# Kernel tuning notes

Measured on AMD Instinct MI355X. Metric: run time of the kernel, lower is better.

The kernel has to match this reference:

```python
import jax, jax.numpy as jnp
import numpy as np

B, T, C, H = 256, 256, 1024, 64

def setup_inputs() -> dict:
    key = jax.random.key(0)
    kx, kk, kq, kv = jax.random.split(key, 4)
    x = jax.random.normal(kx, (B, T, C), dtype=jnp.float32)
    # Dense kernels init'd with normal(stddev=0.02), stored as [in, out] like flax
    Wk = jax.random.normal(kk, (C, H), dtype=jnp.float32) * 0.02
    Wq = jax.random.normal(kq, (C, H), dtype=jnp.float32) * 0.02
    Wv = jax.random.normal(kv, (C, H), dtype=jnp.float32) * 0.02
    return {"x": x, "Wk": Wk, "Wq": Wq, "Wv": Wv}

def reference(x, Wk, Wq, Wv):
    # single-head causal self-attention (eval mode: dropout is identity)
    k = jnp.einsum('btc,ch->bth', x, Wk)      # [B,T,H]
    q = jnp.einsum('btc,ch->bth', x, Wq)      # [B,T,H]
    v = jnp.einsum('btc,ch->bth', x, Wv)      # [B,T,H]
    scale = jnp.asarray(k.shape[-1], k.dtype) ** -0.5
    wei = jnp.einsum('bth,bsh->bts', q, k) * scale  # [B,T,T]
    t = x.shape[1]
    causal = jnp.tril(jnp.ones((t, t), dtype=bool))
    wei = jnp.where(causal, wei, -jnp.inf)
    wei = jax.nn.softmax(wei, axis=-1)
    out = jnp.einsum('bts,bsh->bth', wei, v)  # [B,T,H]
    return out
```

## Files before the change

kernel.cpp:

```cpp
#include <hip/hip_runtime.h>

typedef float f32x4 __attribute__((ext_vector_type(4)));
typedef short s16x8 __attribute__((ext_vector_type(8)));

#define MFMA16 __builtin_amdgcn_mfma_f32_16x16x32_bf16

typedef const __attribute__((address_space(1))) void* gptr_t;
typedef __attribute__((address_space(3))) void* lptr_t;

__device__ __forceinline__ unsigned short f2bf(float f) {
    union { float f; unsigned u; } v; v.f = f;
    unsigned r = v.u + 0x7FFF + ((v.u >> 16) & 1);
    return (unsigned short)(r >> 16);
}

__global__ void prep_w(const float* __restrict__ Wk, const float* __restrict__ Wq,
                       const float* __restrict__ Wv, unsigned short* __restrict__ wt) {
    int n = blockIdx.x;
    int tid = threadIdx.x;
    const float* src; int col; float sc = 1.0f;
    if (n < 64)       { src = Wq; col = n;       sc = 0.125f; }
    else if (n < 128) { src = Wk; col = n - 64; }
    else              { src = Wv; col = n - 128; }
#pragma unroll
    for (int i = 0; i < 4; i++) {
        int c = i * 256 + tid;
        wt[n * 1024 + c] = f2bf(src[c * 64 + col] * sc);
    }
}

__global__ __launch_bounds__(512, 2) void fused_kernel(const float* __restrict__ x,
                                                       const unsigned short* __restrict__ wt,
                                                       float* __restrict__ out) {
    __shared__ unsigned short smem[2 * 256 * 72 + 64 * 264 + 8 * 16 * 56];
    unsigned short* Ql  = smem;
    unsigned short* Kl  = smem + 256 * 72;
    unsigned short* Vt  = smem + 2 * 256 * 72;
    unsigned short* Pl8 = smem + 2 * 256 * 72 + 64 * 264;
    unsigned short* Wl  = smem;

    const int tid  = threadIdx.x;
    const int lane = tid & 63;
    const int wid  = tid >> 6;
    const int quad = lane >> 4;
    const int l15  = lane & 15;
    const int b    = blockIdx.x;
    const int m0   = wid * 32;

    const float* xb  = x + (long)b * 256 * 1024;
    const float* ar0 = xb + (long)(m0 + l15) * 1024 + quad * 8;
    const float* ar1 = ar0 + 16 * 1024;

    const int srow = wid * 24 + (lane >> 3);
    const int cswz = (lane & 7) ^ (srow & 7);

    const unsigned short* wbase0 = Wl + l15 * 64 + ((0 + quad) ^ (l15 & 7)) * 8;
    const unsigned short* wbase1 = Wl + l15 * 64 + ((4 + quad) ^ (l15 & 7)) * 8;

    f32x4 acc[2][12] = {};

    for (int t = 0; t < 16; t++) {
        const int k0 = t * 64;
        if (t) __syncthreads();
#pragma unroll
        for (int j = 0; j < 3; j++) {
            const unsigned short* src = wt + (long)(srow + j * 8) * 1024 + k0 + cswz * 8;
            unsigned short* dst = Wl + (wid * 24 + j * 8) * 64;
            __builtin_amdgcn_global_load_lds((gptr_t)src, (lptr_t)dst, 16, 0, 0);
        }
        float4 px0 = *(const float4*)(ar0 + k0);
        float4 px1 = *(const float4*)(ar0 + k0 + 4);
        float4 px2 = *(const float4*)(ar0 + k0 + 32);
        float4 px3 = *(const float4*)(ar0 + k0 + 36);
        float4 px4 = *(const float4*)(ar1 + k0);
        float4 px5 = *(const float4*)(ar1 + k0 + 4);
        float4 px6 = *(const float4*)(ar1 + k0 + 32);
        float4 px7 = *(const float4*)(ar1 + k0 + 36);
        __syncthreads();

#pragma unroll
        for (int kk = 0; kk < 64; kk += 32) {
            s16x8 bfv[12];
            const unsigned short* wb = (kk == 0) ? wbase0 : wbase1;
#pragma unroll
            for (int nt = 0; nt < 12; nt++)
                bfv[nt] = *(const s16x8*)(wb + nt * 1024);

            s16x8 af0, af1;
            if (kk == 0) {
                af0 = s16x8{ (short)f2bf(px0.x), (short)f2bf(px0.y), (short)f2bf(px0.z), (short)f2bf(px0.w),
                             (short)f2bf(px1.x), (short)f2bf(px1.y), (short)f2bf(px1.z), (short)f2bf(px1.w) };
                af1 = s16x8{ (short)f2bf(px4.x), (short)f2bf(px4.y), (short)f2bf(px4.z), (short)f2bf(px4.w),
                             (short)f2bf(px5.x), (short)f2bf(px5.y), (short)f2bf(px5.z), (short)f2bf(px5.w) };
            } else {
                af0 = s16x8{ (short)f2bf(px2.x), (short)f2bf(px2.y), (short)f2bf(px2.z), (short)f2bf(px2.w),
                             (short)f2bf(px3.x), (short)f2bf(px3.y), (short)f2bf(px3.z), (short)f2bf(px3.w) };
                af1 = s16x8{ (short)f2bf(px6.x), (short)f2bf(px6.y), (short)f2bf(px6.z), (short)f2bf(px6.w),
                             (short)f2bf(px7.x), (short)f2bf(px7.y), (short)f2bf(px7.z), (short)f2bf(px7.w) };
            }
#pragma unroll
            for (int nt = 0; nt < 12; nt++) {
                acc[0][nt] = MFMA16(af0, bfv[nt], acc[0][nt], 0, 0, 0);
                acc[1][nt] = MFMA16(af1, bfv[nt], acc[1][nt], 0, 0, 0);
            }
        }
    }
    __syncthreads();

#pragma unroll
    for (int mt = 0; mt < 2; mt++) {
#pragma unroll
        for (int nt = 0; nt < 12; nt++) {
            if (nt < 4) {
#pragma unroll
                for (int r = 0; r < 4; r++)
                    Ql[(m0 + mt * 16 + quad * 4 + r) * 72 + nt * 16 + l15] = f2bf(acc[mt][nt][r]);
            } else if (nt < 8) {
#pragma unroll
                for (int r = 0; r < 4; r++)
                    Kl[(m0 + mt * 16 + quad * 4 + r) * 72 + (nt - 4) * 16 + l15] = f2bf(acc[mt][nt][r]);
            } else {
                ushort4 pv;
                pv.x = f2bf(acc[mt][nt][0]); pv.y = f2bf(acc[mt][nt][1]);
                pv.z = f2bf(acc[mt][nt][2]); pv.w = f2bf(acc[mt][nt][3]);
                *(ushort4*)&Vt[((nt - 8) * 16 + l15) * 264 + m0 + mt * 16 + quad * 4] = pv;
            }
        }
    }
    __syncthreads();

    unsigned short* Pw = Pl8 + wid * (16 * 56);

#pragma unroll
    for (int ti = 0; ti < 2; ti++) {
        const int r0 = (ti == 0 ? wid : 15 - wid) * 16;

        s16x8 qf0 = *(const s16x8*)&Ql[(r0 + l15) * 72 + quad * 8];
        s16x8 qf1 = *(const s16x8*)&Ql[(r0 + l15) * 72 + 32 + quad * 8];

        f32x4 o[4] = {};
        float mr[4], lr[4];
#pragma unroll
        for (int r = 0; r < 4; r++) { mr[r] = -1e30f; lr[r] = 0.0f; }

        const int nst = (r0 >> 5) + 1;
        for (int st = 0; st < nst; st++) {
            const int s0 = st * 32;
            s16x8 kf00 = *(const s16x8*)&Kl[(s0 + l15) * 72 + quad * 8];
            s16x8 kf01 = *(const s16x8*)&Kl[(s0 + l15) * 72 + 32 + quad * 8];
            s16x8 kf10 = *(const s16x8*)&Kl[(s0 + 16 + l15) * 72 + quad * 8];
            s16x8 kf11 = *(const s16x8*)&Kl[(s0 + 16 + l15) * 72 + 32 + quad * 8];
            s16x8 vf[4];
#pragma unroll
            for (int n = 0; n < 4; n++)
                vf[n] = *(const s16x8*)&Vt[(n * 16 + l15) * 264 + s0 + quad * 8];

            f32x4 S0 = {0.f, 0.f, 0.f, 0.f}, S1 = {0.f, 0.f, 0.f, 0.f};
            S0 = MFMA16(qf0, kf00, S0, 0, 0, 0);
            S0 = MFMA16(qf1, kf01, S0, 0, 0, 0);
            S1 = MFMA16(qf0, kf10, S1, 0, 0, 0);
            S1 = MFMA16(qf1, kf11, S1, 0, 0, 0);

            if (s0 + 31 > r0) {
#pragma unroll
                for (int r = 0; r < 4; r++) {
                    int t = r0 + quad * 4 + r;
                    if (s0 + l15 > t)      S0[r] = -1e30f;
                    if (s0 + 16 + l15 > t) S1[r] = -1e30f;
                }
            }

            float a4[4];
#pragma unroll
            for (int r = 0; r < 4; r++) {
                float rm = fmaxf(S0[r], S1[r]);
                rm = fmaxf(rm, __shfl_xor(rm, 1));
                rm = fmaxf(rm, __shfl_xor(rm, 2));
                rm = fmaxf(rm, __shfl_xor(rm, 4));
                rm = fmaxf(rm, __shfl_xor(rm, 8));
                float mn = fmaxf(mr[r], rm);
                float al = exp2f((mr[r] - mn) * 1.44269504f);
                mr[r] = mn;
                float p0 = exp2f((S0[r] - mn) * 1.44269504f);
                float p1 = exp2f((S1[r] - mn) * 1.44269504f);
                float rs = p0 + p1;
                rs += __shfl_xor(rs, 1);
                rs += __shfl_xor(rs, 2);
                rs += __shfl_xor(rs, 4);
                rs += __shfl_xor(rs, 8);
                lr[r] = al * lr[r] + rs;
                a4[r] = al;
                Pw[(quad * 4 + r) * 56 + l15]      = f2bf(p0);
                Pw[(quad * 4 + r) * 56 + l15 + 16] = f2bf(p1);
            }
#pragma unroll
            for (int n = 0; n < 4; n++) {
                f32x4 tt = o[n];
#pragma unroll
                for (int r = 0; r < 4; r++) tt[r] *= a4[r];
                o[n] = tt;
            }
            s16x8 pf = *(const s16x8*)&Pw[l15 * 56 + quad * 8];
#pragma unroll
            for (int n = 0; n < 4; n++)
                o[n] = MFMA16(pf, vf[n], o[n], 0, 0, 0);
        }

        float inv[4];
#pragma unroll
        for (int r = 0; r < 4; r++) inv[r] = 1.0f / lr[r];
#pragma unroll
        for (int n = 0; n < 4; n++)
#pragma unroll
            for (int r = 0; r < 4; r++) {
                long t = (long)b * 256 + r0 + quad * 4 + r;
                out[t * 64 + n * 16 + l15] = o[n][r] * inv[r];
            }
    }
}

extern "C" void kernel_launch(void* const* d_in, const int* in_sizes, int n_in,
                              void* d_out, int out_size, void* d_ws, size_t ws_size,
                              hipStream_t stream) {
    const float* x  = (const float*)d_in[0];
    const float* Wk = (const float*)d_in[1];
    const float* Wq = (const float*)d_in[2];
    const float* Wv = (const float*)d_in[3];
    float* out = (float*)d_out;

    unsigned short* wt = (unsigned short*)d_ws;

    prep_w<<<192, 256, 0, stream>>>(Wk, Wq, Wv, wt);
    fused_kernel<<<256, 512, 0, stream>>>(x, wt, out);
}
```

Baseline: 409.4 us.

## Software-pipeline projection GEMM with triple-buffered weight tiles and prefetched x

Measured after the change: 409.5 us. About the same (+0.0%).

```diff
diff --git a/kernel.cpp b/kernel.cpp
--- a/kernel.cpp
+++ b/kernel.cpp
@@ -37,7 +37,10 @@
     unsigned short* Kl  = smem + 256 * 72;
     unsigned short* Vt  = smem + 2 * 256 * 72;
     unsigned short* Pl8 = smem + 2 * 256 * 72 + 64 * 264;
-    unsigned short* Wl  = smem;
+    unsigned short* const Wb0 = smem;
+    unsigned short* const Wb1 = smem + 12288;
+    unsigned short* const Wb2 = smem + 24576;
+    unsigned short* const Wb[3] = { Wb0, Wb1, Wb2 };
 
     const int tid  = threadIdx.x;
     const int lane = tid & 63;
@@ -52,52 +55,60 @@
     const float* ar1 = ar0 + 16 * 1024;
 
     const int srow = wid * 24 + (lane >> 3);
-    const int cswz = (lane & 7) ^ (srow & 7);
-
-    const unsigned short* wbase0 = Wl + l15 * 64 + ((0 + quad) ^ (l15 & 7)) * 8;
-    const unsigned short* wbase1 = Wl + l15 * 64 + ((4 + quad) ^ (l15 & 7)) * 8;
+    const int cswz = (lane & 7) ^ (lane >> 3);
+
+    const int woff0 = l15 * 64 + ((0 + quad) ^ (l15 & 7)) * 8;
+    const int woff1 = l15 * 64 + ((4 + quad) ^ (l15 & 7)) * 8;
 
     f32x4 acc[2][12] = {};
-
+    float4 px[2][8];
+
+    auto issueStage = [&](int t, unsigned short* Wd) {
+        const unsigned short* s0 = wt + (long)srow * 1024 + t * 64 + cswz * 8;
+#pragma unroll
+        for (int j = 0; j < 3; j++)
+            __builtin_amdgcn_global_load_lds((gptr_t)(s0 + j * 8 * 1024),
+                                             (lptr_t)(Wd + (wid * 24 + j * 8) * 64), 16, 0, 0);
+    };
+    auto issueX = [&](int t, float4* p) {
+        const int k0 = t * 64;
+        p[0] = *(const float4*)(ar0 + k0);      p[1] = *(const float4*)(ar0 + k0 + 4);
+        p[2] = *(const float4*)(ar0 + k0 + 32); p[3] = *(const float4*)(ar0 + k0 + 36);
+        p[4] = *(const float4*)(ar1 + k0);      p[5] = *(const float4*)(ar1 + k0 + 4);
+        p[6] = *(const float4*)(ar1 + k0 + 32); p[7] = *(const float4*)(ar1 + k0 + 36);
+    };
+
+    issueStage(0, Wb0);
+    issueX(0, px[0]);
+
+#pragma unroll
     for (int t = 0; t < 16; t++) {
-        const int k0 = t * 64;
-        if (t) __syncthreads();
-#pragma unroll
-        for (int j = 0; j < 3; j++) {
-            const unsigned short* src = wt + (long)(srow + j * 8) * 1024 + k0 + cswz * 8;
-            unsigned short* dst = Wl + (wid * 24 + j * 8) * 64;
-            __builtin_amdgcn_global_load_lds((gptr_t)src, (lptr_t)dst, 16, 0, 0);
-        }
-        float4 px0 = *(const float4*)(ar0 + k0);
-        float4 px1 = *(const float4*)(ar0 + k0 + 4);
-        float4 px2 = *(const float4*)(ar0 + k0 + 32);
-        float4 px3 = *(const float4*)(ar0 + k0 + 36);
-        float4 px4 = *(const float4*)(ar1 + k0);
-        float4 px5 = *(const float4*)(ar1 + k0 + 4);
-        float4 px6 = *(const float4*)(ar1 + k0 + 32);
-        float4 px7 = *(const float4*)(ar1 + k0 + 36);
-        __syncthreads();
-
-#pragma unroll
-        for (int kk = 0; kk < 64; kk += 32) {
+        if (t < 15) {
+            issueStage(t + 1, Wb[(t + 1) % 3]);
+            issueX(t + 1, px[(t + 1) & 1]);
+        }
+        __builtin_amdgcn_sched_barrier(0);
+        if (t < 15) asm volatile("s_waitcnt vmcnt(11)" ::: "memory");
+        else        asm volatile("s_waitcnt vmcnt(0)"  ::: "memory");
+        __builtin_amdgcn_s_barrier();
+        __builtin_amdgcn_sched_barrier(0);
+
+        const unsigned short* Wd = Wb[t % 3];
+        float4* p = px[t & 1];
+#pragma unroll
+        for (int kk = 0; kk < 2; kk++) {
+            const unsigned short* wbp = Wd + (kk ? woff1 : woff0);
             s16x8 bfv[12];
-            const unsigned short* wb = (kk == 0) ? wbase0 : wbase1;
 #pragma unroll
             for (int nt = 0; nt < 12; nt++)
-                bfv[nt] = *(const s16x8*)(wb + nt * 1024);
-
-            s16x8 af0, af1;
-            if (kk == 0) {
-                af0 = s16x8{ (short)f2bf(px0.x), (short)f2bf(px0.y), (short)f2bf(px0.z), (short)f2bf(px0.w),
-                             (short)f2bf(px1.x), (short)f2bf(px1.y), (short)f2bf(px1.z), (short)f2bf(px1.w) };
-                af1 = s16x8{ (short)f2bf(px4.x), (short)f2bf(px4.y), (short)f2bf(px4.z), (short)f2bf(px4.w),
-                             (short)f2bf(px5.x), (short)f2bf(px5.y), (short)f2bf(px5.z), (short)f2bf(px5.w) };
-            } else {
-                af0 = s16x8{ (short)f2bf(px2.x), (short)f2bf(px2.y), (short)f2bf(px2.z), (short)f2bf(px2.w),
-                             (short)f2bf(px3.x), (short)f2bf(px3.y), (short)f2bf(px3.z), (short)f2bf(px3.w) };
-                af1 = s16x8{ (short)f2bf(px6.x), (short)f2bf(px6.y), (short)f2bf(px6.z), (short)f2bf(px6.w),
-                             (short)f2bf(px7.x), (short)f2bf(px7.y), (short)f2bf(px7.z), (short)f2bf(px7.w) };
-            }
+                bfv[nt] = *(const s16x8*)(wbp + nt * 1024);
+
+            const float4 a0 = p[kk * 2 + 0], a1 = p[kk * 2 + 1];
+            const float4 a2 = p[kk * 2 + 4], a3 = p[kk * 2 + 5];
+            s16x8 af0 = { (short)f2bf(a0.x), (short)f2bf(a0.y), (short)f2bf(a0.z), (short)f2bf(a0.w),
+                          (short)f2bf(a1.x), (short)f2bf(a1.y), (short)f2bf(a1.z), (short)f2bf(a1.w) };
+            s16x8 af1 = { (short)f2bf(a2.x), (short)f2bf(a2.y), (short)f2bf(a2.z), (short)f2bf(a2.w),
+                          (short)f2bf(a3.x), (short)f2bf(a3.y), (short)f2bf(a3.z), (short)f2bf(a3.w) };
 #pragma unroll
             for (int nt = 0; nt < 12; nt++) {
                 acc[0][nt] = MFMA16(af0, bfv[nt], acc[0][nt], 0, 0, 0);
```
